# Optimization experiments

Hardware: AMD Instinct MI355X
Metric: run time of the kernel (lower is better)

## Reference

```python
import jax, jax.numpy as jnp
import numpy as np

B, L, C, H, W = 2, 8, 64, 128, 128
HID = 256


def setup_inputs() -> dict:
    key = jax.random.key(0)
    k0, k1, k2, k3, k4 = jax.random.split(key, 5)
    x = jax.random.normal(k0, (B, L, C, H, W), dtype=jnp.float32)
    # Conv2d(in*4 -> hidden, kernel=1): weight stored as [out, in] for 1x1
    conv_w = jax.random.normal(k1, (HID, 4 * C), dtype=jnp.float32) * (1.0 / np.sqrt(4 * C))
    conv_b = jax.random.normal(k2, (HID,), dtype=jnp.float32) * 0.01
    conv_out_w = jax.random.normal(k3, (4 * C, HID), dtype=jnp.float32) * (1.0 / np.sqrt(HID))
    conv_out_b = jax.random.normal(k4, (4 * C,), dtype=jnp.float32) * 0.01
    return {"x": x, "conv_w": conv_w, "conv_b": conv_b,
            "conv_out_w": conv_out_w, "conv_out_b": conv_out_b}


def _dwt(x):  # x: [N, C, Hp, Wp] (even dims) -> [N, 4C, Hp/2, Wp/2]
    x1 = x[:, :, 0::2, 0::2] * 0.5
    x2 = x[:, :, 1::2, 0::2] * 0.5
    x3 = x[:, :, 0::2, 1::2] * 0.5
    x4 = x[:, :, 1::2, 1::2] * 0.5
    return jnp.concatenate([x1 + x2 + x3 + x4,
                            -x1 - x2 + x3 + x4,
                            -x1 + x2 - x3 + x4,
                            x1 - x2 - x3 + x4], axis=1)


def _idwt(y):  # y: [N, 4C, Hh, Wh] -> [N, C, 2Hh, 2Wh]
    n, c4, hh, wh = y.shape
    co = c4 // 4
    y1 = y[:, 0 * co:1 * co] * 0.5
    y2 = y[:, 1 * co:2 * co] * 0.5
    y3 = y[:, 2 * co:3 * co] * 0.5
    y4 = y[:, 3 * co:4 * co] * 0.5
    a = y1 - y2 - y3 + y4   # h[0::2, 0::2]
    b = y1 - y2 + y3 - y4   # h[1::2, 0::2]
    c = y1 + y2 - y3 - y4   # h[0::2, 1::2]
    d = y1 + y2 + y3 + y4   # h[1::2, 1::2]
    r0 = jnp.stack([a, c], axis=-1).reshape(n, co, hh, 2 * wh)  # even rows
    r1 = jnp.stack([b, d], axis=-1).reshape(n, co, hh, 2 * wh)  # odd rows
    return jnp.stack([r0, r1], axis=-2).reshape(n, co, 2 * hh, 2 * wh)


def reference(x, conv_w, conv_b, conv_out_w, conv_out_b):
    b, l, c, h, w = x.shape
    pad_h = (2 - h % 2) % 2
    pad_w = (2 - w % 2) % 2
    if pad_h > 0 or pad_w > 0:
        x = jnp.pad(x, ((0, 0), (0, 0), (0, 0), (0, pad_h), (0, pad_w)))
    hp, wp = x.shape[-2], x.shape[-1]
    xf = x.reshape(b * l, c, hp, wp)
    x_dwt = _dwt(xf)                                       # [BL, 4C, hp/2, wp/2]
    feat = jnp.einsum('nchw,oc->nohw', x_dwt, conv_w) + conv_b[None, :, None, None]
    feat = jax.nn.silu(feat)
    y = jnp.einsum('nchw,oc->nohw', feat, conv_out_w) + conv_out_b[None, :, None, None]
    rec = _idwt(y)                                         # [BL, C, hp, wp]
    out = rec.reshape(b, l, c, hp, wp)
    if pad_h > 0 or pad_w > 0:
        out = out[..., :h, :w]
    return out
```

## Files before the change

kernel.cpp:

```cpp
#include <hip/hip_runtime.h>
#include <hip/hip_bf16.h>


typedef __bf16 bf16x8 __attribute__((ext_vector_type(8)));
typedef float  f32x4  __attribute__((ext_vector_type(4)));

#define SP 264

__device__ __forceinline__ void barrier_lds() {
  asm volatile("s_waitcnt lgkmcnt(0)\n\ts_barrier" ::: "memory");
}

__device__ __forceinline__ unsigned short f2bf(float f) {
  __hip_bfloat16 h = __float2bfloat16(f);
  return __builtin_bit_cast(unsigned short, h);
}
__device__ __forceinline__ float bf2f(unsigned short s) {
  union { unsigned int i; float f; } v; v.i = ((unsigned int)s) << 16; return v.f;
}
__device__ __forceinline__ float silu(float f) {
  return f / (1.0f + __expf(-f));
}
__device__ __forceinline__ bf16x8 ldw8(const float* __restrict__ p) {
  const float4 a = *(const float4*)p;
  const float4 b = *(const float4*)(p + 4);
  bf16x8 r;
  r[0] = (__bf16)a.x; r[1] = (__bf16)a.y; r[2] = (__bf16)a.z; r[3] = (__bf16)a.w;
  r[4] = (__bf16)b.x; r[5] = (__bf16)b.y; r[6] = (__bf16)b.z; r[7] = (__bf16)b.w;
  return r;
}

__global__ __launch_bounds__(256) void cvt_w(const float* __restrict__ w1,
                                             const float* __restrict__ w2,
                                             unsigned short* __restrict__ o) {
  const int i = (blockIdx.x * 256 + threadIdx.x) * 4;
  const float4 a = *(const float4*)(w1 + i);
  const float4 b = *(const float4*)(w2 + i);
  *(ushort4*)(o + i)         = make_ushort4(f2bf(a.x), f2bf(a.y), f2bf(a.z), f2bf(a.w));
  *(ushort4*)(o + 65536 + i) = make_ushort4(f2bf(b.x), f2bf(b.y), f2bf(b.z), f2bf(b.w));
}

__device__ __forceinline__ void load_st(const float* __restrict__ x, int n, int hh,
                                        int ww, int cg, float2 (&st)[32]) {
  const float* xb = x + ((size_t)n * 64 * 128 + (size_t)(2 * hh)) * 128 + 2 * ww;
  #pragma unroll
  for (int j = 0; j < 4; ++j) {
    const int c0 = (cg + 4 * j) * 4;
    #pragma unroll
    for (int ci = 0; ci < 4; ++ci) {
      const float* p = xb + (size_t)(c0 + ci) * (128 * 128);
      st[(j * 4 + ci) * 2]     = *(const float2*)p;
      st[(j * 4 + ci) * 2 + 1] = *(const float2*)(p + 128);
    }
  }
}

__device__ __forceinline__ void dwt_write(const float2 (&st)[32], unsigned short* lds,
                                          int ww, int cg) {
  #pragma unroll
  for (int j = 0; j < 4; ++j) {
    const int c0 = (cg + 4 * j) * 4;
    float qv[4][4];
    #pragma unroll
    for (int ci = 0; ci < 4; ++ci) {
      const float2 r0 = st[(j * 4 + ci) * 2];
      const float2 r1 = st[(j * 4 + ci) * 2 + 1];
      const float x1 = r0.x, x3 = r0.y;
      const float x2 = r1.x, x4 = r1.y;
      qv[0][ci] = 0.5f * ((x1 + x2) + (x3 + x4));
      qv[1][ci] = 0.5f * ((x3 + x4) - (x1 + x2));
      qv[2][ci] = 0.5f * ((x2 + x4) - (x1 + x3));
      qv[3][ci] = 0.5f * ((x1 + x4) - (x2 + x3));
    }
    #pragma unroll
    for (int q = 0; q < 4; ++q) {
      ushort4 v = make_ushort4(f2bf(qv[q][0]), f2bf(qv[q][1]), f2bf(qv[q][2]), f2bf(qv[q][3]));
      *(ushort4*)(&lds[ww * SP + q * 64 + c0]) = v;
    }
  }
}

template <bool WBF16>
__device__ __forceinline__ void process_row(unsigned short* lds,
                                            const void* __restrict__ w1p,
                                            const float* __restrict__ b1,
                                            const void* __restrict__ w2p,
                                            const float* __restrict__ b2,
                                            float* __restrict__ out, int n, int hh,
                                            int t, int ww, int cg) {
  const int wv   = t >> 6;
  const int r    = t & 15;
  const int quad = (t & 63) >> 4;

  {
    f32x4 acc[4][4];
    #pragma unroll
    for (int mt = 0; mt < 4; ++mt)
      #pragma unroll
      for (int nt = 0; nt < 4; ++nt)
        acc[mt][nt] = (f32x4){0.0f, 0.0f, 0.0f, 0.0f};

    #pragma unroll
    for (int k0 = 0; k0 < 256; k0 += 32) {
      bf16x8 a[4], b[4];
      #pragma unroll
      for (int mt = 0; mt < 4; ++mt) {
        const int row = wv * 64 + mt * 16 + r;
        if constexpr (WBF16)
          a[mt] = *(const bf16x8*)((const unsigned short*)w1p + row * 256 + quad * 8 + k0);
        else
          a[mt] = ldw8((const float*)w1p + row * 256 + quad * 8 + k0);
      }
      #pragma unroll
      for (int nt = 0; nt < 4; ++nt)
        b[nt] = *(const bf16x8*)(&lds[(nt * 16 + r) * SP + quad * 8 + k0]);
      #pragma unroll
      for (int mt = 0; mt < 4; ++mt)
        #pragma unroll
        for (int nt = 0; nt < 4; ++nt)
          acc[mt][nt] = __builtin_amdgcn_mfma_f32_16x16x32_bf16(a[mt], b[nt], acc[mt][nt], 0, 0, 0);
    }
    barrier_lds();

    #pragma unroll
    for (int mt = 0; mt < 4; ++mt) {
      const int ob = wv * 64 + mt * 16 + quad * 4;
      const float4 bb = *(const float4*)(b1 + ob);
      #pragma unroll
      for (int nt = 0; nt < 4; ++nt) {
        const int pix = nt * 16 + r;
        ushort4 v;
        v.x = f2bf(silu(acc[mt][nt][0] + bb.x));
        v.y = f2bf(silu(acc[mt][nt][1] + bb.y));
        v.z = f2bf(silu(acc[mt][nt][2] + bb.z));
        v.w = f2bf(silu(acc[mt][nt][3] + bb.w));
        *(ushort4*)(&lds[pix * SP + ob]) = v;
      }
    }
  }
  barrier_lds();

  {
    f32x4 acc[4][4];
    #pragma unroll
    for (int mt = 0; mt < 4; ++mt)
      #pragma unroll
      for (int nt = 0; nt < 4; ++nt)
        acc[mt][nt] = (f32x4){0.0f, 0.0f, 0.0f, 0.0f};

    #pragma unroll
    for (int k0 = 0; k0 < 256; k0 += 32) {
      bf16x8 a[4], b[4];
      #pragma unroll
      for (int mt = 0; mt < 4; ++mt) {
        const int row = wv * 64 + mt * 16 + r;
        if constexpr (WBF16)
          a[mt] = *(const bf16x8*)((const unsigned short*)w2p + row * 256 + quad * 8 + k0);
        else
          a[mt] = ldw8((const float*)w2p + row * 256 + quad * 8 + k0);
      }
      #pragma unroll
      for (int nt = 0; nt < 4; ++nt)
        b[nt] = *(const bf16x8*)(&lds[(nt * 16 + r) * SP + quad * 8 + k0]);
      #pragma unroll
      for (int mt = 0; mt < 4; ++mt)
        #pragma unroll
        for (int nt = 0; nt < 4; ++nt)
          acc[mt][nt] = __builtin_amdgcn_mfma_f32_16x16x32_bf16(a[mt], b[nt], acc[mt][nt], 0, 0, 0);
    }
    barrier_lds();

    #pragma unroll
    for (int mt = 0; mt < 4; ++mt) {
      const int cb = wv * 64 + mt * 16 + quad * 4;
      const float4 bb = *(const float4*)(b2 + cb);
      #pragma unroll
      for (int nt = 0; nt < 4; ++nt) {
        const int pix = nt * 16 + r;
        ushort4 v;
        v.x = f2bf(acc[mt][nt][0] + bb.x);
        v.y = f2bf(acc[mt][nt][1] + bb.y);
        v.z = f2bf(acc[mt][nt][2] + bb.z);
        v.w = f2bf(acc[mt][nt][3] + bb.w);
        *(ushort4*)(&lds[pix * SP + cb]) = v;
      }
    }
  }
  barrier_lds();

  {
    float* ob_ = out + ((size_t)n * 64 * 128 + (size_t)(2 * hh)) * 128 + 2 * ww;
    #pragma unroll
    for (int j = 0; j < 4; ++j) {
      const int c0 = (cg + 4 * j) * 4;
      unsigned short yb[4][4];
      #pragma unroll
      for (int q = 0; q < 4; ++q) {
        const ushort4 v = *(const ushort4*)(&lds[ww * SP + q * 64 + c0]);
        yb[q][0] = v.x; yb[q][1] = v.y; yb[q][2] = v.z; yb[q][3] = v.w;
      }
      #pragma unroll
      for (int ci = 0; ci < 4; ++ci) {
        const float y1 = 0.5f * bf2f(yb[0][ci]);
        const float y2 = 0.5f * bf2f(yb[1][ci]);
        const float y3 = 0.5f * bf2f(yb[2][ci]);
        const float y4 = 0.5f * bf2f(yb[3][ci]);
        const float s14 = y1 + y4, s23 = y2 + y3;
        const float d14 = y1 - y4, d23 = y2 - y3;
        const float oa  = s14 - s23;
        const float oc  = d14 + d23;
        const float obv = d14 - d23;
        const float od  = s14 + s23;
        float* prow = ob_ + (size_t)(c0 + ci) * (128 * 128);
        *(float2*)prow         = make_float2(oa, oc);
        *(float2*)(prow + 128) = make_float2(obv, od);
      }
    }
  }
}

template <bool WBF16>
__global__ __launch_bounds__(256, 2)
void wavelet_fused(const float* __restrict__ x,
                   const void* __restrict__ w1p,
                   const float* __restrict__ b1,
                   const void* __restrict__ w2p,
                   const float* __restrict__ b2,
                   float* __restrict__ out)
{
  __shared__ unsigned short lds[64 * SP];

  const int t  = threadIdx.x;
  const int ww = t & 63;
  const int cg = t >> 6;

  const int idx0 = blockIdx.x;
  const int idx1 = blockIdx.x + 512;
  const int n0 = idx0 >> 6, hh0 = idx0 & 63;
  const int n1 = idx1 >> 6, hh1 = idx1 & 63;

  float2 st[32];

  load_st(x, n0, hh0, ww, cg, st);
  dwt_write(st, lds, ww, cg);
  barrier_lds();

  load_st(x, n1, hh1, ww, cg, st);

  process_row<WBF16>(lds, w1p, b1, w2p, b2, out, n0, hh0, t, ww, cg);

  barrier_lds();
  dwt_write(st, lds, ww, cg);
  barrier_lds();

  process_row<WBF16>(lds, w1p, b1, w2p, b2, out, n1, hh1, t, ww, cg);
}

extern "C" void kernel_launch(void* const* d_in, const int* in_sizes, int n_in,
                              void* d_out, int out_size, void* d_ws, size_t ws_size,
                              hipStream_t stream) {
  (void)in_sizes; (void)n_in; (void)out_size;
  const float* x  = (const float*)d_in[0];
  const float* w1 = (const float*)d_in[1];
  const float* b1 = (const float*)d_in[2];
  const float* w2 = (const float*)d_in[3];
  const float* b2 = (const float*)d_in[4];
  float* o = (float*)d_out;

  if (ws_size >= 2u * 65536u * sizeof(unsigned short)) {
    unsigned short* wb = (unsigned short*)d_ws;
    cvt_w<<<dim3(64), dim3(256), 0, stream>>>(w1, w2, wb);
    wavelet_fused<true><<<dim3(512), dim3(256), 0, stream>>>(
        x, wb, b1, wb + 65536, b2, o);
  } else {
    wavelet_fused<false><<<dim3(512), dim3(256), 0, stream>>>(
        x, w1, b1, w2, b2, o);
  }
}
```

Before: 147.1 us.

## Widen DWT global loads/stores to float4 and remap blocks across XCDs

Each thread now covers two output columns and eight channels, so global loads and the IDWT stores use float4 instead of float2, and LDS writes and reads use 16-byte vectors instead of 8-byte ones. The block-to-(n,row) mapping is also changed so that the eight XCDs each get a contiguous band of row indices, which is meant to improve L2 locality. The aim is fewer memory instructions and better cache behaviour on a bandwidth-bound kernel. The wider LDS row accesses may cause more bank conflicts.

```diff
diff --git a/kernel.cpp b/kernel.cpp
--- a/kernel.cpp
+++ b/kernel.cpp
@@ -4,6 +4,7 @@
 
 typedef __bf16 bf16x8 __attribute__((ext_vector_type(8)));
 typedef float  f32x4  __attribute__((ext_vector_type(4)));
+typedef unsigned short u16x8 __attribute__((ext_vector_type(8)));
 
 #define SP 264
 
@@ -41,43 +42,40 @@
 }
 
 __device__ __forceinline__ void load_st(const float* __restrict__ x, int n, int hh,
-                                        int ww, int cg, float2 (&st)[32]) {
-  const float* xb = x + ((size_t)n * 64 * 128 + (size_t)(2 * hh)) * 128 + 2 * ww;
+                                        int u, int g, float4 (&st)[16]) {
+  const float* xb = x + ((size_t)n * 64 * 128 + (size_t)(2 * hh)) * 128 + 4 * u;
   #pragma unroll
-  for (int j = 0; j < 4; ++j) {
-    const int c0 = (cg + 4 * j) * 4;
-    #pragma unroll
-    for (int ci = 0; ci < 4; ++ci) {
-      const float* p = xb + (size_t)(c0 + ci) * (128 * 128);
-      st[(j * 4 + ci) * 2]     = *(const float2*)p;
-      st[(j * 4 + ci) * 2 + 1] = *(const float2*)(p + 128);
-    }
-  }
-}
-
-__device__ __forceinline__ void dwt_write(const float2 (&st)[32], unsigned short* lds,
-                                          int ww, int cg) {
+  for (int i = 0; i < 8; ++i) {
+    const float* p = xb + (size_t)(g * 8 + i) * (128 * 128);
+    st[2 * i]     = *(const float4*)p;
+    st[2 * i + 1] = *(const float4*)(p + 128);
+  }
+}
+
+__device__ __forceinline__ void dwt_write(const float4 (&st)[16], unsigned short* lds,
+                                          int u, int g) {
+  u16x8 v[4][2];
   #pragma unroll
-  for (int j = 0; j < 4; ++j) {
-    const int c0 = (cg + 4 * j) * 4;
-    float qv[4][4];
-    #pragma unroll
-    for (int ci = 0; ci < 4; ++ci) {
-      const float2 r0 = st[(j * 4 + ci) * 2];
-      const float2 r1 = st[(j * 4 + ci) * 2 + 1];
-      const float x1 = r0.x, x3 = r0.y;
-      const float x2 = r1.x, x4 = r1.y;
-      qv[0][ci] = 0.5f * ((x1 + x2) + (x3 + x4));
-      qv[1][ci] = 0.5f * ((x3 + x4) - (x1 + x2));
-      qv[2][ci] = 0.5f * ((x2 + x4) - (x1 + x3));
-      qv[3][ci] = 0.5f * ((x1 + x4) - (x2 + x3));
-    }
-    #pragma unroll
-    for (int q = 0; q < 4; ++q) {
-      ushort4 v = make_ushort4(f2bf(qv[q][0]), f2bf(qv[q][1]), f2bf(qv[q][2]), f2bf(qv[q][3]));
-      *(ushort4*)(&lds[ww * SP + q * 64 + c0]) = v;
-    }
-  }
+  for (int i = 0; i < 8; ++i) {
+    const float4 r0 = st[2 * i];
+    const float4 r1 = st[2 * i + 1];
+    #pragma unroll
+    for (int p = 0; p < 2; ++p) {
+      const float x1 = p ? r0.z : r0.x;
+      const float x3 = p ? r0.w : r0.y;
+      const float x2 = p ? r1.z : r1.x;
+      const float x4 = p ? r1.w : r1.y;
+      v[0][p][i] = f2bf(0.5f * ((x1 + x2) + (x3 + x4)));
+      v[1][p][i] = f2bf(0.5f * ((x3 + x4) - (x1 + x2)));
+      v[2][p][i] = f2bf(0.5f * ((x2 + x4) - (x1 + x3)));
+      v[3][p][i] = f2bf(0.5f * ((x1 + x4) - (x2 + x3)));
+    }
+  }
+  #pragma unroll
+  for (int p = 0; p < 2; ++p)
+    #pragma unroll
+    for (int q = 0; q < 4; ++q)
+      *(u16x8*)(&lds[(2 * u + p) * SP + q * 64 + g * 8]) = v[q][p];
 }
 
 template <bool WBF16>
@@ -87,7 +85,7 @@
                                             const void* __restrict__ w2p,
                                             const float* __restrict__ b2,
                                             float* __restrict__ out, int n, int hh,
-                                            int t, int ww, int cg) {
+                                            int t, int u, int g) {
   const int wv   = t >> 6;
   const int r    = t & 15;
   const int quad = (t & 63) >> 4;
@@ -189,32 +187,30 @@
   barrier_lds();
 
   {
-    float* ob_ = out + ((size_t)n * 64 * 128 + (size_t)(2 * hh)) * 128 + 2 * ww;
-    #pragma unroll
-    for (int j = 0; j < 4; ++j) {
-      const int c0 = (cg + 4 * j) * 4;
-      unsigned short yb[4][4];
-      #pragma unroll
-      for (int q = 0; q < 4; ++q) {
-        const ushort4 v = *(const ushort4*)(&lds[ww * SP + q * 64 + c0]);
-        yb[q][0] = v.x; yb[q][1] = v.y; yb[q][2] = v.z; yb[q][3] = v.w;
-      }
-      #pragma unroll
-      for (int ci = 0; ci < 4; ++ci) {
-        const float y1 = 0.5f * bf2f(yb[0][ci]);
-        const float y2 = 0.5f * bf2f(yb[1][ci]);
-        const float y3 = 0.5f * bf2f(yb[2][ci]);
-        const float y4 = 0.5f * bf2f(yb[3][ci]);
+    float* ob_ = out + ((size_t)n * 64 * 128 + (size_t)(2 * hh)) * 128 + 4 * u;
+    u16x8 yq[2][4];
+    #pragma unroll
+    for (int p = 0; p < 2; ++p)
+      #pragma unroll
+      for (int q = 0; q < 4; ++q)
+        yq[p][q] = *(const u16x8*)(&lds[(2 * u + p) * SP + q * 64 + g * 8]);
+    #pragma unroll
+    for (int i = 0; i < 8; ++i) {
+      float4 e, o;
+      #pragma unroll
+      for (int p = 0; p < 2; ++p) {
+        const float y1 = 0.5f * bf2f(yq[p][0][i]);
+        const float y2 = 0.5f * bf2f(yq[p][1][i]);
+        const float y3 = 0.5f * bf2f(yq[p][2][i]);
+        const float y4 = 0.5f * bf2f(yq[p][3][i]);
         const float s14 = y1 + y4, s23 = y2 + y3;
         const float d14 = y1 - y4, d23 = y2 - y3;
-        const float oa  = s14 - s23;
-        const float oc  = d14 + d23;
-        const float obv = d14 - d23;
-        const float od  = s14 + s23;
-        float* prow = ob_ + (size_t)(c0 + ci) * (128 * 128);
-        *(float2*)prow         = make_float2(oa, oc);
-        *(float2*)(prow + 128) = make_float2(obv, od);
-      }
+        if (p == 0) { e.x = s14 - s23; e.y = d14 + d23; o.x = d14 - d23; o.y = s14 + s23; }
+        else        { e.z = s14 - s23; e.w = d14 + d23; o.z = d14 - d23; o.w = s14 + s23; }
+      }
+      float* prow = ob_ + (size_t)(g * 8 + i) * (128 * 128);
+      *(float4*)prow         = e;
+      *(float4*)(prow + 128) = o;
     }
   }
 }
@@ -230,30 +226,31 @@
 {
   __shared__ unsigned short lds[64 * SP];
 
-  const int t  = threadIdx.x;
-  const int ww = t & 63;
-  const int cg = t >> 6;
-
-  const int idx0 = blockIdx.x;
-  const int idx1 = blockIdx.x + 512;
-  const int n0 = idx0 >> 6, hh0 = idx0 & 63;
-  const int n1 = idx1 >> 6, hh1 = idx1 & 63;
-
-  float2 st[32];
-
-  load_st(x, n0, hh0, ww, cg, st);
-  dwt_write(st, lds, ww, cg);
-  barrier_lds();
-
-  load_st(x, n1, hh1, ww, cg, st);
-
-  process_row<WBF16>(lds, w1p, b1, w2p, b2, out, n0, hh0, t, ww, cg);
-
-  barrier_lds();
-  dwt_write(st, lds, ww, cg);
-  barrier_lds();
-
-  process_row<WBF16>(lds, w1p, b1, w2p, b2, out, n1, hh1, t, ww, cg);
+  const int t = threadIdx.x;
+  const int u = t & 31;
+  const int g = t >> 5;
+
+  const int xcd = blockIdx.x & 7;
+  const int k   = blockIdx.x >> 3;
+  const int n0  = k & 7;
+  const int hh  = (xcd << 3) | (k >> 3);
+  const int n1  = n0 + 8;
+
+  float4 st[16];
+
+  load_st(x, n0, hh, u, g, st);
+  dwt_write(st, lds, u, g);
+  barrier_lds();
+
+  load_st(x, n1, hh, u, g, st);
+
+  process_row<WBF16>(lds, w1p, b1, w2p, b2, out, n0, hh, t, u, g);
+
+  barrier_lds();
+  dwt_write(st, lds, u, g);
+  barrier_lds();
+
+  process_row<WBF16>(lds, w1p, b1, w2p, b2, out, n1, hh, t, u, g);
 }
 
 extern "C" void kernel_launch(void* const* d_in, const int* in_sizes, int n_in,
```

Result: no change. 145.7 us (median of 2 runs) (-1.0%).
